# Kernel optimization log

Hardware: AMD Instinct MI355X
Metric: run time of the kernel (lower is better)

The kernel has to match this reference:

```python
import jax, jax.numpy as jnp
import numpy as np

B, N, E = 32, 2048, 65536
SLOPE = 0.01  # torch LeakyReLU default

def _lrelu(x):
    return jax.nn.leaky_relu(x, SLOPE)

def setup_inputs() -> dict:
    key = jax.random.key(0)
    ks = jax.random.split(key, 32)
    def w(k, shape):
        return jax.random.normal(k, shape, dtype=jnp.float32) * 0.1
    inp = {}
    inp['vertices'] = jax.random.normal(ks[0], (B, N, 11), dtype=jnp.float32)
    inp['edges'] = jax.random.randint(ks[1], (2, E), 0, N, dtype=jnp.int32)
    # x/y/th pairwise feature extractors: Conv2d(1,8,kernel=(1,2)) == linear 2->8
    inp['Wx'], inp['bx'] = w(ks[2], (8, 2)), w(ks[3], (8,))
    inp['Wy'], inp['by'] = w(ks[4], (8, 2)), w(ks[5], (8,))
    inp['Wth'], inp['bth'] = w(ks[6], (8, 2)), w(ks[7], (8,))
    # config_lin: 24->32, 32->32 (1x1 convs)
    inp['W1c'], inp['b1c'] = w(ks[8], (32, 24)), w(ks[9], (32,))
    inp['W2c'], inp['b2c'] = w(ks[10], (32, 32)), w(ks[11], (32,))
    # vertex_lin: 64->32, 32->32
    inp['W1v'], inp['b1v'] = w(ks[12], (32, 64)), w(ks[13], (32,))
    inp['W2v'], inp['b2v'] = w(ks[14], (32, 32)), w(ks[15], (32,))
    # edge_lin: Conv2d(1,32,kernel=(68,1)) == linear 68->32, then 32->32
    inp['W1e'], inp['b1e'] = w(ks[16], (32, 68)), w(ks[17], (32,))
    inp['W2e'], inp['b2e'] = w(ks[18], (32, 32)), w(ks[19], (32,))
    # vertex_output_lin: Conv2d(1,32,kernel=(32,1)) == linear 32->32, then 32->1
    inp['W1o'], inp['b1o'] = w(ks[20], (32, 32)), w(ks[21], (32,))
    inp['W2o'], inp['b2o'] = w(ks[22], (1, 32)), w(ks[23], (1,))
    # graph_output_lin: Linear(N, 1)
    inp['Wg'], inp['bg'] = w(ks[24], (1, N)) * 0.1, w(ks[25], (1,))
    return inp

def _pair_feat(a, b, W, bb):
    # a, b: [B,N] -> [B,N,2] @ W.T -> [B,N,8]
    p = jnp.stack([a, b], axis=-1)
    return _lrelu(p @ W.T + bb)

def reference(vertices, edges, Wx, bx, Wy, by, Wth, bth, W1c, b1c, W2c, b2c,
              W1v, b1v, W2v, b2v, W1e, b1e, W2e, b2e, W1o, b1o, W2o, b2o, Wg, bg):
    qk = vertices[:, :, 0:3]
    q0 = vertices[:, :, 3:6]
    qg = vertices[:, :, 6:9]
    col = vertices[:, :, 9:11]  # [B,N,2]

    def config_feat(qa, qb):
        fx = _pair_feat(qa[..., 0], qb[..., 0], Wx, bx)
        fy = _pair_feat(qa[..., 1], qb[..., 1], Wy, by)
        fth = _pair_feat(qa[..., 2], qb[..., 2], Wth, bth)
        c = jnp.concatenate([fx, fy, fth], axis=-1)  # [B,N,24]
        h = _lrelu(c @ W1c.T + b1c)
        return _lrelu(h @ W2c.T + b2c)  # [B,N,32]

    cf = jnp.concatenate([config_feat(qk, q0), config_feat(qk, qg)], axis=-1)  # [B,N,64]
    vf = _lrelu(cf @ W1v.T + b1v)
    vf = _lrelu(vf @ W2v.T + b2v)  # [B,N,32]
    vf = jnp.concatenate([vf, col], axis=-1)  # [B,N,34]

    src, dst = edges[0], edges[1]
    pair = jnp.concatenate([vf[:, src, :], vf[:, dst, :]], axis=-1)  # [B,E,68]
    m = jax.nn.relu(pair @ W1e.T + b1e)
    m = _lrelu(m @ W2e.T + b2e)  # [B,E,32]

    n_nodes = vertices.shape[1]
    sums = jnp.zeros((vertices.shape[0], n_nodes, m.shape[-1]), m.dtype).at[:, dst, :].add(m)
    cnt = jnp.zeros((n_nodes,), m.dtype).at[dst].add(1.0)
    agg = sums / jnp.maximum(cnt, 1.0)[None, :, None]  # scatter_mean; empty bins -> 0

    fv = jax.nn.relu(agg @ W1o.T + b1o)
    fv = _lrelu(fv @ W2o.T + b2o)[..., 0]  # [B,N]
    return jax.nn.sigmoid(fv @ Wg.T + bg)  # [B,1]
```

## Files before the change

kernel.cpp:

```cpp
#include <hip/hip_runtime.h>
#include <hip/hip_fp16.h>
#include <math.h>

constexpr int B = 32;
constexpr int NN = 2048;
constexpr int E = 65536;
constexpr float SLOPE = 0.01f;

typedef __attribute__((ext_vector_type(8))) _Float16 f16x8;
typedef __attribute__((ext_vector_type(4))) float f32x4;

__device__ __forceinline__ float lrelu(float x) { return fmaxf(x, SLOPE * x); }
__device__ __forceinline__ int imin(int a, int b) { return a < b ? a : b; }
__device__ __forceinline__ int imax(int a, int b) { return a > b ? a : b; }

__device__ __forceinline__ unsigned int cvtpk(float lo, float hi) {
    unsigned int r;
    asm("v_cvt_pk_bf16_f32 %0, %1, %2" : "=v"(r) : "v"(lo), "v"(hi));
    return r;
}
__device__ __forceinline__ unsigned int pkrtz(float lo, float hi) {
    unsigned int r;
    asm("v_cvt_pkrtz_f16_f32 %0, %1, %2" : "=v"(r) : "v"(lo), "v"(hi));
    return r;
}
__device__ __forceinline__ unsigned int pk_addrelu(unsigned int a, unsigned int b) {
    unsigned int s, r;
    asm("v_pk_add_f16 %0, %1, %2" : "=v"(s) : "v"(a), "v"(b));
    asm("v_pk_max_f16 %0, %1, %2" : "=v"(r) : "v"(s), "v"(0u));
    return r;
}

__device__ __forceinline__ void unpack_bf16(unsigned int u, float& lo, float& hi) {
    lo = __uint_as_float(u << 16);
    hi = __uint_as_float(u & 0xffff0000u);
}

__device__ __forceinline__ void unpack8(const uint4& u, float f[8]) {
    unpack_bf16(u.x, f[0], f[1]);
    unpack_bf16(u.y, f[2], f[3]);
    unpack_bf16(u.z, f[4], f[5]);
    unpack_bf16(u.w, f[6], f[7]);
}

union UH8 { unsigned int u[4]; uint4 q; f16x8 v; };

__device__ __forceinline__ void fma_grp16(const float* __restrict__ Wt, int jj, int o0,
                                          const uint4& r, float acc[16]) {
    float x[8]; unpack8(r, x);
    const float* Wp = Wt + jj * 256 + o0;
    #pragma unroll
    for (int jo = 0; jo < 8; ++jo) {
        #pragma unroll
        for (int o = 0; o < 16; ++o) acc[o] += x[jo] * Wp[jo * 32 + o];
    }
}

__device__ __forceinline__ void layerN16(const unsigned short* col, int G, int o0,
                                         const float* __restrict__ Wt, float acc[16]) {
    uint4 cur = *(const uint4*)col;
    #pragma unroll 1
    for (int jj = 0; jj < G; ++jj) {
        uint4 nxt = (jj + 1 < G) ? *(const uint4*)(col + (jj + 1) * 8) : cur;
        fma_grp16(Wt, jj, o0, cur, acc);
        cur = nxt;
    }
}

__device__ __forceinline__ void layer2N16(const unsigned short* col, int G, int o0,
                                          const float* __restrict__ Ws,
                                          const float* __restrict__ Wd,
                                          float a1[16], float a2[16]) {
    uint4 cur = *(const uint4*)col;
    #pragma unroll 1
    for (int jj = 0; jj < G; ++jj) {
        uint4 nxt = (jj + 1 < G) ? *(const uint4*)(col + (jj + 1) * 8) : cur;
        float x[8]; unpack8(cur, x);
        const float* Wps = Ws + jj * 256 + o0;
        const float* Wpd = Wd + jj * 256 + o0;
        #pragma unroll
        for (int jo = 0; jo < 8; ++jo) {
            #pragma unroll
            for (int o = 0; o < 16; ++o) a1[o] += x[jo] * Wps[jo * 32 + o];
            #pragma unroll
            for (int o = 0; o < 16; ++o) a2[o] += x[jo] * Wpd[jo * 32 + o];
        }
        cur = nxt;
    }
}

__global__ __launch_bounds__(256) void prep_zero_kernel(
    const float* __restrict__ W1c, const float* __restrict__ W2c,
    const float* __restrict__ W1v, const float* __restrict__ W2v,
    const float* __restrict__ W1e, const float* __restrict__ W2e,
    const float* __restrict__ W1o,
    float* __restrict__ W1cT, float* __restrict__ W2cT,
    float* __restrict__ W1vT, float* __restrict__ W2vT,
    float* __restrict__ W1sT, float* __restrict__ W1dT,
    unsigned short* __restrict__ W2eh, unsigned short* __restrict__ W1oTh,
    int* __restrict__ cnt, int* __restrict__ cursor)
{
    int blk = blockIdx.x;
    if (blk < 8) {
        int i = blk * 256 + threadIdx.x;
        cnt[i] = 0;
        cursor[i] = 0;
        return;
    }
    int t = (blk - 8) * 256 + threadIdx.x;
    for (int i = t; i < 32 * 24; i += 1024) W1cT[(i % 24) * 32 + i / 24] = W1c[i];
    for (int i = t; i < 32 * 32; i += 1024) W2cT[(i % 32) * 32 + i / 32] = W2c[i];
    for (int i = t; i < 32 * 64; i += 1024) W1vT[(i % 64) * 32 + i / 64] = W1v[i];
    for (int i = t; i < 32 * 32; i += 1024) W2vT[(i % 32) * 32 + i / 32] = W2v[i];
    for (int i = t; i < 32 * 68; i += 1024) {
        int o = i / 68, j = i % 68;
        if (j < 34) W1sT[j * 32 + o] = W1e[i];
        else        W1dT[(j - 34) * 32 + o] = W1e[i];
    }
    for (int i = t; i < 32 * 32; i += 1024) {
        __half hv = __float2half(W2e[i]);
        W2eh[i] = __half_as_ushort(hv);
    }
    for (int i = t; i < 512; i += 1024) {
        int o = i >> 4, m = i & 15;
        W1oTh[o * 32 + 2 * m]     = __half_as_ushort(__float2half(W1o[o * 32 + m]));
        W1oTh[o * 32 + 2 * m + 1] = __half_as_ushort(__float2half(W1o[o * 32 + 16 + m]));
    }
}

__global__ __launch_bounds__(256) void count_kernel(const int* __restrict__ edges, int* __restrict__ cnt)
{
    int e = blockIdx.x * 256 + threadIdx.x;
    if (e < E) atomicAdd(&cnt[edges[E + e]], 1);
}

__global__ __launch_bounds__(1024) void scan_kernel(const int* __restrict__ cnt, int* __restrict__ offs)
{
    __shared__ int s[1024];
    int t = threadIdx.x;
    int c0 = cnt[2 * t], c1 = cnt[2 * t + 1];
    int own = c0 + c1;
    s[t] = own;
    __syncthreads();
    int v = own;
    for (int d = 1; d < 1024; d <<= 1) {
        int add = (t >= d) ? s[t - d] : 0;
        __syncthreads();
        v += add;
        s[t] = v;
        __syncthreads();
    }
    int excl = v - own;
    offs[2 * t] = excl;
    offs[2 * t + 1] = excl + c0;
    if (t == 1023) offs[2048] = v;
}

__global__ __launch_bounds__(256) void fill_kernel(
    const int* __restrict__ edges, const int* __restrict__ offs,
    int* __restrict__ cursor, int* __restrict__ elist)
{
    int e = blockIdx.x * 256 + threadIdx.x;
    if (e < E) {
        int d = edges[E + e];
        int p = atomicAdd(&cursor[d], 1);
        elist[offs[d] + p] = edges[e];
    }
}

__global__ __launch_bounds__(256) void vertex_kernel(
    const float* __restrict__ vert,
    const float* __restrict__ Wx,  const float* __restrict__ bx,
    const float* __restrict__ Wy,  const float* __restrict__ by,
    const float* __restrict__ Wth, const float* __restrict__ bth,
    const float* __restrict__ b1c, const float* __restrict__ b2c,
    const float* __restrict__ b1v, const float* __restrict__ b2v,
    const float* __restrict__ b1e,
    const float* __restrict__ W1cT, const float* __restrict__ W2cT,
    const float* __restrict__ W1vT, const float* __restrict__ W2vT,
    const float* __restrict__ W1sT, const float* __restrict__ W1dT,
    unsigned int* __restrict__ asrc, unsigned int* __restrict__ adst)
{
    __shared__ unsigned short bufS[128 * 40];
    __shared__ unsigned short bufT[128 * 40];
    __shared__ unsigned short bufC[128 * 72];
    int tid = threadIdx.x;
    int w = tid >> 6, lane = tid & 63;
    int g = w >> 1;
    int h = w & 1;
    int o0 = __builtin_amdgcn_readfirstlane(h << 4);
    int nl = g * 64 + lane;
    int idx = blockIdx.x * 128 + nl;
    unsigned short* Sc = bufS + nl * 40;
    unsigned short* Tc = bufT + nl * 40;
    unsigned short* Cc = bufC + nl * 72;

    const float* v = vert + (size_t)idx * 11;
    float qk0 = v[0], qk1 = v[1], qk2 = v[2];
    float q00 = v[3], q01 = v[4], q02 = v[5];
    float qg0 = v[6], qg1 = v[7], qg2 = v[8];
    float col0 = v[9], col1 = v[10];

    for (int cfh = 0; cfh < 2; ++cfh) {
        float a0 = cfh ? qg0 : q00;
        float a1 = cfh ? qg1 : q01;
        float a2 = cfh ? qg2 : q02;
        if (h == 0) {
            #pragma unroll
            for (int i = 0; i < 4; ++i) {
                ((unsigned int*)Sc)[i] = cvtpk(
                    lrelu(qk0 * Wx[4 * i]     + a0 * Wx[4 * i + 1] + bx[2 * i]),
                    lrelu(qk0 * Wx[4 * i + 2] + a0 * Wx[4 * i + 3] + bx[2 * i + 1]));
                ((unsigned int*)Sc)[4 + i] = cvtpk(
                    lrelu(qk1 * Wy[4 * i]     + a1 * Wy[4 * i + 1] + by[2 * i]),
                    lrelu(qk1 * Wy[4 * i + 2] + a1 * Wy[4 * i + 3] + by[2 * i + 1]));
            }
        } else {
            #pragma unroll
            for (int i = 0; i < 4; ++i) {
                ((unsigned int*)Sc)[8 + i] = cvtpk(
                    lrelu(qk2 * Wth[4 * i]     + a2 * Wth[4 * i + 1] + bth[2 * i]),
                    lrelu(qk2 * Wth[4 * i + 2] + a2 * Wth[4 * i + 3] + bth[2 * i + 1]));
            }
        }
        __syncthreads();

        float hh[16];
        #pragma unroll
        for (int o = 0; o < 16; ++o) hh[o] = b1c[o0 + o];
        layerN16(Sc, 3, o0, W1cT, hh);
        #pragma unroll
        for (int q = 0; q < 8; ++q)
            ((unsigned int*)Tc)[h * 8 + q] = cvtpk(lrelu(hh[2 * q]), lrelu(hh[2 * q + 1]));
        __syncthreads();

        float gg[16];
        #pragma unroll
        for (int o = 0; o < 16; ++o) gg[o] = b2c[o0 + o];
        layerN16(Tc, 4, o0, W2cT, gg);
        #pragma unroll
        for (int q = 0; q < 8; ++q)
            ((unsigned int*)Cc)[cfh * 16 + h * 8 + q] =
                cvtpk(lrelu(gg[2 * q]), lrelu(gg[2 * q + 1]));
        __syncthreads();
    }

    float v1[16];
    #pragma unroll
    for (int o = 0; o < 16; ++o) v1[o] = b1v[o0 + o];
    layerN16(Cc, 8, o0, W1vT, v1);
    #pragma unroll
    for (int q = 0; q < 8; ++q)
        ((unsigned int*)Sc)[h * 8 + q] = cvtpk(lrelu(v1[2 * q]), lrelu(v1[2 * q + 1]));
    __syncthreads();

    float v2[16];
    #pragma unroll
    for (int o = 0; o < 16; ++o) v2[o] = b2v[o0 + o];
    layerN16(Sc, 4, o0, W2vT, v2);
    #pragma unroll
    for (int q = 0; q < 8; ++q)
        ((unsigned int*)Tc)[h * 8 + q] = cvtpk(lrelu(v2[2 * q]), lrelu(v2[2 * q + 1]));
    __syncthreads();

    float as[16], ad[16];
    #pragma unroll
    for (int o = 0; o < 16; ++o) { as[o] = 0.f; ad[o] = b1e[o0 + o]; }
    layer2N16(Tc, 4, o0, W1sT, W1dT, as, ad);
    #pragma unroll
    for (int o = 0; o < 16; ++o) {
        as[o] += col0 * W1sT[32 * 32 + o0 + o] + col1 * W1sT[33 * 32 + o0 + o];
        ad[o] += col0 * W1dT[32 * 32 + o0 + o] + col1 * W1dT[33 * 32 + o0 + o];
    }

    unsigned int* ps = asrc + ((size_t)idx << 4) + h * 8;
    unsigned int* pd = adst + ((size_t)idx << 4) + h * 8;
    #pragma unroll
    for (int q = 0; q < 8; ++q) {
        ps[q] = pkrtz(as[2 * q], as[2 * q + 1]);
        pd[q] = pkrtz(ad[2 * q], ad[2 * q + 1]);
    }
}

__device__ __forceinline__ void chunk_step(
    const uint4* __restrict__ abq, const int* __restrict__ elist,
    int e0, int end, int e1, int col, int grp,
    uint4& su_c, int& src_n, const uint4& adr,
    const UH8& Bf0, const UH8& Bf1, float bias0, float bias1,
    float& s0, float& s1)
{
    uint4 su_n = abq[(src_n << 2) | grp];
    int src_n2 = elist[imin(e0 + 32 + col, e1)];

    UH8 A;
    A.u[0] = pk_addrelu(su_c.x, adr.x);
    A.u[1] = pk_addrelu(su_c.y, adr.y);
    A.u[2] = pk_addrelu(su_c.z, adr.z);
    A.u[3] = pk_addrelu(su_c.w, adr.w);
    if ((e0 + col) >= end) {
        A.u[0] = 0; A.u[1] = 0; A.u[2] = 0; A.u[3] = 0;
    }

    f32x4 acc0 = {bias0, bias0, bias0, bias0};
    f32x4 acc1 = {bias1, bias1, bias1, bias1};
    acc0 = __builtin_amdgcn_mfma_f32_16x16x32_f16(A.v, Bf0.v, acc0, 0, 0, 0);
    acc1 = __builtin_amdgcn_mfma_f32_16x16x32_f16(A.v, Bf1.v, acc1, 0, 0, 0);

    #pragma unroll
    for (int r = 0; r < 4; ++r) {
        s0 += lrelu(acc0[r]);
        s1 += lrelu(acc1[r]);
    }
    su_c = su_n;
    src_n = src_n2;
}

__global__ __launch_bounds__(512) void edge_kernel(
    const unsigned int* __restrict__ asrc, const unsigned int* __restrict__ adst,
    const int* __restrict__ elist, const int* __restrict__ offs,
    const unsigned short* __restrict__ W2eh, const float* __restrict__ b2e,
    const unsigned short* __restrict__ W1oTh, const float* __restrict__ b1o,
    const float* __restrict__ W2o,  const float* __restrict__ b2o,
    float* __restrict__ fv)
{
    __shared__ unsigned int aggbuf[8 * 16 * 20];
    int logical = (blockIdx.x & 7) * 64 + (blockIdx.x >> 3);
    int b = logical >> 4;
    int seg = logical & 15;
    int tid = threadIdx.x;
    int wv = tid >> 6;
    int lane = tid & 63;
    int col = lane & 15;
    int grp = lane >> 4;

    const uint4* abq = (const uint4*)(asrc + (((size_t)b * NN) << 4));
    unsigned int* wvagg = aggbuf + wv * (16 * 20);

    UH8 Bf0, Bf1;
    Bf0.q = *(const uint4*)(W2eh + col * 32 + grp * 8);
    Bf1.q = *(const uint4*)(W2eh + (col + 16) * 32 + grp * 8);
    UH8 Bo0, Bo1;
    Bo0.q = *(const uint4*)(W1oTh + col * 32 + grp * 8);
    Bo1.q = *(const uint4*)(W1oTh + (col + 16) * 32 + grp * 8);
    float bias0 = b2e[col];
    float bias1 = b2e[col + 16];
    float lb0 = lrelu(bias0);
    float lb1 = lrelu(bias1);
    float b1o_lo = b1o[col];
    float b1o_hi = b1o[col + 16];
    float w2o_lo = W2o[col];
    float w2o_hi = W2o[col + 16];
    float b2oc = b2o[0];
    const unsigned int* adb = adst + (((size_t)b * NN) << 4) + grp * 4;

    int dbase = seg * 128 + wv * 16;
    for (int dp = 0; dp < 8; ++dp) {
        int dA = dbase + 2 * dp;
        int dB = dA + 1;
        int startA = offs[dA];
        int endA = offs[dB];
        int endB = offs[dB + 1];
        int startB = endA;
        int degA = endA - startA;
        int degB = endB - startB;
        int e1A = imax(endA - 1, 0);
        int e1B = imax(endB - 1, 0);

        const uint4 adrA = *(const uint4*)(adb + ((size_t)dA << 4));
        const uint4 adrB = *(const uint4*)(adb + ((size_t)dB << 4));

        int n = imax((degA + 15) >> 4, (degB + 15) >> 4);

        float s0A = 0.f, s1A = 0.f, s0B = 0.f, s1B = 0.f;
        if (n > 0) {
            int srcA = elist[imin(startA + col, e1A)];
            int srcB = elist[imin(startB + col, e1B)];
            uint4 suA = abq[(srcA << 2) | grp];
            uint4 suB = abq[(srcB << 2) | grp];
            int srcnA = elist[imin(startA + 16 + col, e1A)];
            int srcnB = elist[imin(startB + 16 + col, e1B)];

            for (int it = 0; it < n; ++it) {
                int e0A = startA + (it << 4);
                int e0B = startB + (it << 4);
                chunk_step(abq, elist, e0A, endA, e1A, col, grp,
                           suA, srcnA, adrA, Bf0, Bf1, bias0, bias1, s0A, s1A);
                chunk_step(abq, elist, e0B, endB, e1B, col, grp,
                           suB, srcnB, adrB, Bf0, Bf1, bias0, bias1, s0B, s1B);
            }
        }

        s0A += __shfl_xor(s0A, 16); s0A += __shfl_xor(s0A, 32);
        s1A += __shfl_xor(s1A, 16); s1A += __shfl_xor(s1A, 32);
        s0B += __shfl_xor(s0B, 16); s0B += __shfl_xor(s0B, 32);
        s1B += __shfl_xor(s1B, 16); s1B += __shfl_xor(s1B, 32);

        float padA = (float)(16 * n - degA);
        float padB = (float)(16 * n - degB);
        s0A -= padA * lb0; s1A -= padA * lb1;
        s0B -= padB * lb0; s1B -= padB * lb1;

        float invA = 1.f / fmaxf((float)degA, 1.f);
        float invB = 1.f / fmaxf((float)degB, 1.f);
        if (grp == 0) {
            wvagg[(2 * dp) * 20 + col]     = pkrtz(s0A * invA, s1A * invA);
            wvagg[(2 * dp + 1) * 20 + col] = pkrtz(s0B * invB, s1B * invB);
        }
    }

    UH8 Ao;
    Ao.q = *(const uint4*)(wvagg + col * 20 + grp * 4);
    f32x4 acc0 = {b1o_lo, b1o_lo, b1o_lo, b1o_lo};
    f32x4 acc1 = {b1o_hi, b1o_hi, b1o_hi, b1o_hi};
    acc0 = __builtin_amdgcn_mfma_f32_16x16x32_f16(Ao.v, Bo0.v, acc0, 0, 0, 0);
    acc1 = __builtin_amdgcn_mfma_f32_16x16x32_f16(Ao.v, Bo1.v, acc1, 0, 0, 0);

    float* fvb = fv + (size_t)b * NN + dbase + grp * 4;
    #pragma unroll
    for (int r = 0; r < 4; ++r) {
        float t = fmaxf(acc0[r], 0.f) * w2o_lo + fmaxf(acc1[r], 0.f) * w2o_hi;
        t += __shfl_xor(t, 1);
        t += __shfl_xor(t, 2);
        t += __shfl_xor(t, 4);
        t += __shfl_xor(t, 8);
        if (col == 0) fvb[r] = lrelu(t + b2oc);
    }
}

__global__ __launch_bounds__(256) void final_kernel(
    const float* __restrict__ fv, const float* __restrict__ Wg,
    const float* __restrict__ bg, float* __restrict__ out)
{
    int b = blockIdx.x;
    int t = threadIdx.x;
    float p = 0.f;
    for (int n = t; n < NN; n += 256) p += fv[(size_t)b * NN + n] * Wg[n];
    __shared__ float red[256];
    red[t] = p;
    __syncthreads();
    for (int s = 128; s > 0; s >>= 1) {
        if (t < s) red[t] += red[t + s];
        __syncthreads();
    }
    if (t == 0) {
        float x = red[0] + bg[0];
        out[b] = 1.f / (1.f + expf(-x));
    }
}

extern "C" void kernel_launch(void* const* d_in, const int* in_sizes, int n_in,
                              void* d_out, int out_size, void* d_ws, size_t ws_size,
                              hipStream_t stream)
{
    const float* vert = (const float*)d_in[0];
    const int*   edges = (const int*)d_in[1];
    const float* Wx  = (const float*)d_in[2];
    const float* bx  = (const float*)d_in[3];
    const float* Wy  = (const float*)d_in[4];
    const float* by  = (const float*)d_in[5];
    const float* Wth = (const float*)d_in[6];
    const float* bth = (const float*)d_in[7];
    const float* W1c = (const float*)d_in[8];
    const float* b1c = (const float*)d_in[9];
    const float* W2c = (const float*)d_in[10];
    const float* b2c = (const float*)d_in[11];
    const float* W1v = (const float*)d_in[12];
    const float* b1v = (const float*)d_in[13];
    const float* W2v = (const float*)d_in[14];
    const float* b2v = (const float*)d_in[15];
    const float* W1e = (const float*)d_in[16];
    const float* b1e = (const float*)d_in[17];
    const float* W2e = (const float*)d_in[18];
    const float* b2e = (const float*)d_in[19];
    const float* W1o = (const float*)d_in[20];
    const float* b1o = (const float*)d_in[21];
    const float* W2o = (const float*)d_in[22];
    const float* b2o = (const float*)d_in[23];
    const float* Wg  = (const float*)d_in[24];
    const float* bg  = (const float*)d_in[25];
    float* out = (float*)d_out;

    char* w = (char*)d_ws;
    unsigned int* asrc = (unsigned int*)w; w += (size_t)B * NN * 32 * 2;
    unsigned int* adst = (unsigned int*)w; w += (size_t)B * NN * 32 * 2;
    float* fv   = (float*)w; w += (size_t)B * NN * 4;
    float* W1cT = (float*)w; w += 32 * 24 * 4;
    float* W2cT = (float*)w; w += 32 * 32 * 4;
    float* W1vT = (float*)w; w += 32 * 64 * 4;
    float* W2vT = (float*)w; w += 32 * 32 * 4;
    float* W1sT = (float*)w; w += 34 * 32 * 4;
    float* W1dT = (float*)w; w += 34 * 32 * 4;
    unsigned short* W2eh  = (unsigned short*)w; w += 32 * 32 * 2;
    unsigned short* W1oTh = (unsigned short*)w; w += 32 * 32 * 2;
    int* cnt    = (int*)w;   w += NN * 4;
    int* cursor = (int*)w;   w += NN * 4;
    int* offs   = (int*)w;   w += 2052 * 4;
    int* elist  = (int*)w;   w += E * 4;

    prep_zero_kernel<<<12, 256, 0, stream>>>(W1c, W2c, W1v, W2v, W1e, W2e, W1o,
                                             W1cT, W2cT, W1vT, W2vT, W1sT, W1dT,
                                             W2eh, W1oTh, cnt, cursor);
    count_kernel<<<E / 256, 256, 0, stream>>>(edges, cnt);
    scan_kernel<<<1, 1024, 0, stream>>>(cnt, offs);
    fill_kernel<<<E / 256, 256, 0, stream>>>(edges, offs, cursor, elist);

    vertex_kernel<<<(B * NN) / 128, 256, 0, stream>>>(
        vert, Wx, bx, Wy, by, Wth, bth, b1c, b2c, b1v, b2v, b1e,
        W1cT, W2cT, W1vT, W2vT, W1sT, W1dT, asrc, adst);

    edge_kernel<<<B * 16, 512, 0, stream>>>(
        asrc, adst, elist, offs, W2eh, b2e, W1oTh, b1o, W2o, b2o, fv);

    final_kernel<<<B, 256, 0, stream>>>(fv, Wg, bg, out);
}
```

Before: 95.52 us.

## Fuse count+scan, fill+vertex, and edge+final kernels to cut launches

Merges the edge-count and prefix-scan kernels into one kernel that uses a last-block ticket, so the final block performs the scan. The CSR fill is folded into the vertex kernel as extra blocks, and the final graph-level reduction is folded into the edge kernel through per-batch atomic accumulation plus a completion counter. This drops from seven kernel launches to four and removes the fv round trip through global memory. In exchange it adds atomics, threadfence-based cross-block synchronization, and a nondeterministic float summation order.

```diff
diff --git a/kernel.cpp b/kernel.cpp
--- a/kernel.cpp
+++ b/kernel.cpp
@@ -98,13 +98,18 @@
     float* __restrict__ W1vT, float* __restrict__ W2vT,
     float* __restrict__ W1sT, float* __restrict__ W1dT,
     unsigned short* __restrict__ W2eh, unsigned short* __restrict__ W1oTh,
-    int* __restrict__ cnt, int* __restrict__ cursor)
+    int* __restrict__ cnt, int* __restrict__ cursor,
+    float* __restrict__ bacc, int* __restrict__ dcnt, int* __restrict__ ticket)
 {
     int blk = blockIdx.x;
     if (blk < 8) {
         int i = blk * 256 + threadIdx.x;
         cnt[i] = 0;
         cursor[i] = 0;
+        if (blk == 0) {
+            if (threadIdx.x < 32) { bacc[threadIdx.x] = 0.f; dcnt[threadIdx.x] = 0; }
+            if (threadIdx.x == 32) ticket[0] = 0;
+        }
         return;
     }
     int t = (blk - 8) * 256 + threadIdx.x;
@@ -117,10 +122,8 @@
         if (j < 34) W1sT[j * 32 + o] = W1e[i];
         else        W1dT[(j - 34) * 32 + o] = W1e[i];
     }
-    for (int i = t; i < 32 * 32; i += 1024) {
-        __half hv = __float2half(W2e[i]);
-        W2eh[i] = __half_as_ushort(hv);
-    }
+    for (int i = t; i < 32 * 32; i += 1024)
+        W2eh[i] = __half_as_ushort(__float2half(W2e[i]));
     for (int i = t; i < 512; i += 1024) {
         int o = i >> 4, m = i & 15;
         W1oTh[o * 32 + 2 * m]     = __half_as_ushort(__float2half(W1o[o * 32 + m]));
@@ -128,17 +131,23 @@
     }
 }
 
-__global__ __launch_bounds__(256) void count_kernel(const int* __restrict__ edges, int* __restrict__ cnt)
-{
-    int e = blockIdx.x * 256 + threadIdx.x;
-    if (e < E) atomicAdd(&cnt[edges[E + e]], 1);
-}
-
-__global__ __launch_bounds__(1024) void scan_kernel(const int* __restrict__ cnt, int* __restrict__ offs)
+__global__ __launch_bounds__(1024) void count_scan_kernel(
+    const int* __restrict__ edges, int* __restrict__ cnt,
+    int* __restrict__ ticket, int* __restrict__ offs)
 {
     __shared__ int s[1024];
+    __shared__ int lastf;
     int t = threadIdx.x;
-    int c0 = cnt[2 * t], c1 = cnt[2 * t + 1];
+    int e = blockIdx.x * 1024 + t;
+    atomicAdd(&cnt[edges[E + e]], 1);
+    __syncthreads();
+    __threadfence();
+    if (t == 0) lastf = (atomicAdd(ticket, 1) == 63);
+    __syncthreads();
+    if (!lastf) return;
+
+    int c0 = atomicAdd(&cnt[2 * t], 0);
+    int c1 = atomicAdd(&cnt[2 * t + 1], 0);
     int own = c0 + c1;
     s[t] = own;
     __syncthreads();
@@ -156,19 +165,9 @@
     if (t == 1023) offs[2048] = v;
 }
 
-__global__ __launch_bounds__(256) void fill_kernel(
+__global__ __launch_bounds__(256) void fill_vertex_kernel(
     const int* __restrict__ edges, const int* __restrict__ offs,
-    int* __restrict__ cursor, int* __restrict__ elist)
-{
-    int e = blockIdx.x * 256 + threadIdx.x;
-    if (e < E) {
-        int d = edges[E + e];
-        int p = atomicAdd(&cursor[d], 1);
-        elist[offs[d] + p] = edges[e];
-    }
-}
-
-__global__ __launch_bounds__(256) void vertex_kernel(
+    int* __restrict__ cursor, int* __restrict__ elist,
     const float* __restrict__ vert,
     const float* __restrict__ Wx,  const float* __restrict__ bx,
     const float* __restrict__ Wy,  const float* __restrict__ by,
@@ -184,13 +183,22 @@
     __shared__ unsigned short bufS[128 * 40];
     __shared__ unsigned short bufT[128 * 40];
     __shared__ unsigned short bufC[128 * 72];
+
+    if (blockIdx.x < 256) {
+        int e = blockIdx.x * 256 + threadIdx.x;
+        int d = edges[E + e];
+        int p = atomicAdd(&cursor[d], 1);
+        elist[offs[d] + p] = edges[e];
+        return;
+    }
+
     int tid = threadIdx.x;
     int w = tid >> 6, lane = tid & 63;
     int g = w >> 1;
     int h = w & 1;
     int o0 = __builtin_amdgcn_readfirstlane(h << 4);
     int nl = g * 64 + lane;
-    int idx = blockIdx.x * 128 + nl;
+    int idx = (blockIdx.x - 256) * 128 + nl;
     unsigned short* Sc = bufS + nl * 40;
     unsigned short* Tc = bufT + nl * 40;
     unsigned short* Cc = bufC + nl * 72;
@@ -315,13 +323,14 @@
     src_n = src_n2;
 }
 
-__global__ __launch_bounds__(512) void edge_kernel(
+__global__ __launch_bounds__(512) void edge_final_kernel(
     const unsigned int* __restrict__ asrc, const unsigned int* __restrict__ adst,
     const int* __restrict__ elist, const int* __restrict__ offs,
     const unsigned short* __restrict__ W2eh, const float* __restrict__ b2e,
     const unsigned short* __restrict__ W1oTh, const float* __restrict__ b1o,
     const float* __restrict__ W2o,  const float* __restrict__ b2o,
-    float* __restrict__ fv)
+    const float* __restrict__ Wg,   const float* __restrict__ bg,
+    float* __restrict__ bacc, int* __restrict__ dcnt, float* __restrict__ out)
 {
     __shared__ unsigned int aggbuf[8 * 16 * 20];
     int logical = (blockIdx.x & 7) * 64 + (blockIdx.x >> 3);
@@ -415,36 +424,27 @@
     acc0 = __builtin_amdgcn_mfma_f32_16x16x32_f16(Ao.v, Bo0.v, acc0, 0, 0, 0);
     acc1 = __builtin_amdgcn_mfma_f32_16x16x32_f16(Ao.v, Bo1.v, acc1, 0, 0, 0);
 
-    float* fvb = fv + (size_t)b * NN + dbase + grp * 4;
+    float p = 0.f;
     #pragma unroll
     for (int r = 0; r < 4; ++r) {
-        float t = fmaxf(acc0[r], 0.f) * w2o_lo + fmaxf(acc1[r], 0.f) * w2o_hi;
-        t += __shfl_xor(t, 1);
-        t += __shfl_xor(t, 2);
-        t += __shfl_xor(t, 4);
-        t += __shfl_xor(t, 8);
-        if (col == 0) fvb[r] = lrelu(t + b2oc);
-    }
-}
-
-__global__ __launch_bounds__(256) void final_kernel(
-    const float* __restrict__ fv, const float* __restrict__ Wg,
-    const float* __restrict__ bg, float* __restrict__ out)
-{
-    int b = blockIdx.x;
-    int t = threadIdx.x;
-    float p = 0.f;
-    for (int n = t; n < NN; n += 256) p += fv[(size_t)b * NN + n] * Wg[n];
-    __shared__ float red[256];
-    red[t] = p;
+        float tt = fmaxf(acc0[r], 0.f) * w2o_lo + fmaxf(acc1[r], 0.f) * w2o_hi;
+        tt += __shfl_xor(tt, 1);
+        tt += __shfl_xor(tt, 2);
+        tt += __shfl_xor(tt, 4);
+        tt += __shfl_xor(tt, 8);
+        if (col == 0) p += lrelu(tt + b2oc) * Wg[dbase + grp * 4 + r];
+    }
+    p += __shfl_xor(p, 16);
+    p += __shfl_xor(p, 32);
+    if (lane == 0) atomicAdd(&bacc[b], p);
+
     __syncthreads();
-    for (int s = 128; s > 0; s >>= 1) {
-        if (t < s) red[t] += red[t + s];
-        __syncthreads();
-    }
-    if (t == 0) {
-        float x = red[0] + bg[0];
-        out[b] = 1.f / (1.f + expf(-x));
+    if (tid == 0) {
+        __threadfence();
+        if (atomicAdd(&dcnt[b], 1) == 15) {
+            float s = atomicAdd(&bacc[b], 0.f);
+            out[b] = 1.f / (1.f + expf(-(s + bg[0])));
+        }
     }
 }
 
@@ -483,7 +483,6 @@
     char* w = (char*)d_ws;
     unsigned int* asrc = (unsigned int*)w; w += (size_t)B * NN * 32 * 2;
     unsigned int* adst = (unsigned int*)w; w += (size_t)B * NN * 32 * 2;
-    float* fv   = (float*)w; w += (size_t)B * NN * 4;
     float* W1cT = (float*)w; w += 32 * 24 * 4;
     float* W2cT = (float*)w; w += 32 * 32 * 4;
     float* W1vT = (float*)w; w += 32 * 64 * 4;
@@ -496,20 +495,23 @@
     int* cursor = (int*)w;   w += NN * 4;
     int* offs   = (int*)w;   w += 2052 * 4;
     int* elist  = (int*)w;   w += E * 4;
+    float* bacc = (float*)w; w += 32 * 4;
+    int* dcnt   = (int*)w;   w += 32 * 4;
+    int* ticket = (int*)w;   w += 4 * 4;
 
     prep_zero_kernel<<<12, 256, 0, stream>>>(W1c, W2c, W1v, W2v, W1e, W2e, W1o,
                                              W1cT, W2cT, W1vT, W2vT, W1sT, W1dT,
-                                             W2eh, W1oTh, cnt, cursor);
-    count_kernel<<<E / 256, 256, 0, stream>>>(edges, cnt);
-    scan_kernel<<<1, 1024, 0, stream>>>(cnt, offs);
-    fill_kernel<<<E / 256, 256, 0, stream>>>(edges, offs, cursor, elist);
-
-    vertex_kernel<<<(B * NN) / 128, 256, 0, stream>>>(
-        vert, Wx, bx, Wy, by, Wth, bth, b1c, b2c, b1v, b2v, b1e,
+                                             W2eh, W1oTh, cnt, cursor,
+                                             bacc, dcnt, ticket);
+
+    count_scan_kernel<<<64, 1024, 0, stream>>>(edges, cnt, ticket, offs);
+
+    fill_vertex_kernel<<<768, 256, 0, stream>>>(
+        edges, offs, cursor, elist, vert,
+        Wx, bx, Wy, by, Wth, bth, b1c, b2c, b1v, b2v, b1e,
         W1cT, W2cT, W1vT, W2vT, W1sT, W1dT, asrc, adst);
 
-    edge_kernel<<<B * 16, 512, 0, stream>>>(
-        asrc, adst, elist, offs, W2eh, b2e, W1oTh, b1o, W2o, b2o, fv);
-
-    final_kernel<<<B, 256, 0, stream>>>(fv, Wg, bg, out);
-}
+    edge_final_kernel<<<B * 16, 512, 0, stream>>>(
+        asrc, adst, elist, offs, W2eh, b2e, W1oTh, b1o, W2o, b2o,
+        Wg, bg, bacc, dcnt, out);
+}
```

After: 124.5 us. 1.3x slower.

## Merge count+scan via last-block ticket and fuse fill into vertex kernel

Applied to the files above, without the earlier changes.

Count and scan are merged into one kernel in which the last block to finish, found through an atomic ticket, performs the prefix scan over the counts. The fill step is folded into the vertex kernel as 256 extra leading blocks, so the CSR fill and the vertex MLP run in the same launch. This cuts the launch count from seven to five and lets the fill overlap vertex work. The cost is a threadfence-and-ticket protocol, and the fill blocks now reserve the vertex kernel's shared memory even though they do not use it.

```diff
diff --git a/kernel.cpp b/kernel.cpp
--- a/kernel.cpp
+++ b/kernel.cpp
@@ -98,13 +98,14 @@
     float* __restrict__ W1vT, float* __restrict__ W2vT,
     float* __restrict__ W1sT, float* __restrict__ W1dT,
     unsigned short* __restrict__ W2eh, unsigned short* __restrict__ W1oTh,
-    int* __restrict__ cnt, int* __restrict__ cursor)
+    int* __restrict__ cnt, int* __restrict__ cursor, int* __restrict__ ticket)
 {
     int blk = blockIdx.x;
     if (blk < 8) {
         int i = blk * 256 + threadIdx.x;
         cnt[i] = 0;
         cursor[i] = 0;
+        if (blk == 0 && threadIdx.x == 0) ticket[0] = 0;
         return;
     }
     int t = (blk - 8) * 256 + threadIdx.x;
@@ -117,10 +118,8 @@
         if (j < 34) W1sT[j * 32 + o] = W1e[i];
         else        W1dT[(j - 34) * 32 + o] = W1e[i];
     }
-    for (int i = t; i < 32 * 32; i += 1024) {
-        __half hv = __float2half(W2e[i]);
-        W2eh[i] = __half_as_ushort(hv);
-    }
+    for (int i = t; i < 32 * 32; i += 1024)
+        W2eh[i] = __half_as_ushort(__float2half(W2e[i]));
     for (int i = t; i < 512; i += 1024) {
         int o = i >> 4, m = i & 15;
         W1oTh[o * 32 + 2 * m]     = __half_as_ushort(__float2half(W1o[o * 32 + m]));
@@ -128,17 +127,23 @@
     }
 }
 
-__global__ __launch_bounds__(256) void count_kernel(const int* __restrict__ edges, int* __restrict__ cnt)
-{
-    int e = blockIdx.x * 256 + threadIdx.x;
-    if (e < E) atomicAdd(&cnt[edges[E + e]], 1);
-}
-
-__global__ __launch_bounds__(1024) void scan_kernel(const int* __restrict__ cnt, int* __restrict__ offs)
+__global__ __launch_bounds__(1024) void count_scan_kernel(
+    const int* __restrict__ edges, int* __restrict__ cnt,
+    int* __restrict__ ticket, int* __restrict__ offs)
 {
     __shared__ int s[1024];
+    __shared__ int lastf;
     int t = threadIdx.x;
-    int c0 = cnt[2 * t], c1 = cnt[2 * t + 1];
+    int e = blockIdx.x * 1024 + t;
+    atomicAdd(&cnt[edges[E + e]], 1);
+    __syncthreads();
+    __threadfence();
+    if (t == 0) lastf = (atomicAdd(ticket, 1) == 63);
+    __syncthreads();
+    if (!lastf) return;
+
+    int c0 = atomicAdd(&cnt[2 * t], 0);
+    int c1 = atomicAdd(&cnt[2 * t + 1], 0);
     int own = c0 + c1;
     s[t] = own;
     __syncthreads();
@@ -156,19 +161,9 @@
     if (t == 1023) offs[2048] = v;
 }
 
-__global__ __launch_bounds__(256) void fill_kernel(
+__global__ __launch_bounds__(256) void fill_vertex_kernel(
     const int* __restrict__ edges, const int* __restrict__ offs,
-    int* __restrict__ cursor, int* __restrict__ elist)
-{
-    int e = blockIdx.x * 256 + threadIdx.x;
-    if (e < E) {
-        int d = edges[E + e];
-        int p = atomicAdd(&cursor[d], 1);
-        elist[offs[d] + p] = edges[e];
-    }
-}
-
-__global__ __launch_bounds__(256) void vertex_kernel(
+    int* __restrict__ cursor, int* __restrict__ elist,
     const float* __restrict__ vert,
     const float* __restrict__ Wx,  const float* __restrict__ bx,
     const float* __restrict__ Wy,  const float* __restrict__ by,
@@ -184,13 +179,22 @@
     __shared__ unsigned short bufS[128 * 40];
     __shared__ unsigned short bufT[128 * 40];
     __shared__ unsigned short bufC[128 * 72];
+
+    if (blockIdx.x < 256) {
+        int e = blockIdx.x * 256 + threadIdx.x;
+        int d = edges[E + e];
+        int p = atomicAdd(&cursor[d], 1);
+        elist[offs[d] + p] = edges[e];
+        return;
+    }
+
     int tid = threadIdx.x;
     int w = tid >> 6, lane = tid & 63;
     int g = w >> 1;
     int h = w & 1;
     int o0 = __builtin_amdgcn_readfirstlane(h << 4);
     int nl = g * 64 + lane;
-    int idx = blockIdx.x * 128 + nl;
+    int idx = (blockIdx.x - 256) * 128 + nl;
     unsigned short* Sc = bufS + nl * 40;
     unsigned short* Tc = bufT + nl * 40;
     unsigned short* Cc = bufC + nl * 72;
@@ -496,16 +500,17 @@
     int* cursor = (int*)w;   w += NN * 4;
     int* offs   = (int*)w;   w += 2052 * 4;
     int* elist  = (int*)w;   w += E * 4;
+    int* ticket = (int*)w;   w += 4 * 4;
 
     prep_zero_kernel<<<12, 256, 0, stream>>>(W1c, W2c, W1v, W2v, W1e, W2e, W1o,
                                              W1cT, W2cT, W1vT, W2vT, W1sT, W1dT,
-                                             W2eh, W1oTh, cnt, cursor);
-    count_kernel<<<E / 256, 256, 0, stream>>>(edges, cnt);
-    scan_kernel<<<1, 1024, 0, stream>>>(cnt, offs);
-    fill_kernel<<<E / 256, 256, 0, stream>>>(edges, offs, cursor, elist);
-
-    vertex_kernel<<<(B * NN) / 128, 256, 0, stream>>>(
-        vert, Wx, bx, Wy, by, Wth, bth, b1c, b2c, b1v, b2v, b1e,
+                                             W2eh, W1oTh, cnt, cursor, ticket);
+
+    count_scan_kernel<<<64, 1024, 0, stream>>>(edges, cnt, ticket, offs);
+
+    fill_vertex_kernel<<<768, 256, 0, stream>>>(
+        edges, offs, cursor, elist, vert,
+        Wx, bx, Wy, by, Wth, bth, b1c, b2c, b1v, b2v, b1e,
         W1cT, W2cT, W1vT, W2vT, W1sT, W1dT, asrc, adst);
 
     edge_kernel<<<B * 16, 512, 0, stream>>>(
```

Measured after the change: 105.1 us. 10.0% more time.
